# Optimization experiments

Measured on AMD Instinct MI355X. Metric: run time of the kernel, lower is better.

The kernel has to match this reference:

```python
import jax, jax.numpy as jnp
import numpy as np
import math

B, S, D, H = 4, 2048, 1024, 16
HD = D // H  # head_dim = 64


def _rope_tables(max_len, half_dim, theta=10000.0):
    inv_freq = 1.0 / (theta ** (jnp.arange(0, half_dim, dtype=jnp.float32) / half_dim))
    ang = jnp.arange(max_len, dtype=jnp.float32)[:, None] * inv_freq[None, :]  # [max_len, half_dim]
    return jnp.cos(ang), jnp.sin(ang)


def _apply_rope(x, cos, sin):
    # x: [B, H, S, HD]; cos/sin: [S, HD/2]
    x1, x2 = x[..., ::2], x[..., 1::2]
    # matches torch.cat([x1*cos - x2*sin, x1*sin + x2*cos], dim=-1)
    return jnp.concatenate([x1 * cos - x2 * sin, x1 * sin + x2 * cos], axis=-1)


def setup_inputs() -> dict:
    key = jax.random.key(0)
    kx, kq, ko = jax.random.split(key, 3)
    x = jax.random.normal(kx, (B, S, D), dtype=jnp.float32)
    Wqkv = jax.random.normal(kq, (D, 3 * D), dtype=jnp.float32) / math.sqrt(D)
    Wout = jax.random.normal(ko, (D, D), dtype=jnp.float32) / math.sqrt(D)
    cos, sin = _rope_tables(S, HD // 2)
    # causal additive mask, per-batch as in module signature [B, S, S]
    causal = jnp.where(jnp.tril(jnp.ones((S, S), dtype=bool)), 0.0, -1e9).astype(jnp.float32)
    mask = jnp.broadcast_to(causal, (B, S, S))
    return {"x": x, "cos": cos, "sin": sin, "mask": mask, "Wqkv": Wqkv, "Wout": Wout}


def reference(x, cos, sin, mask, Wqkv, Wout):
    b, s, d = x.shape
    qkv = x @ Wqkv  # [B, S, 3D]
    q, k, v = jnp.split(qkv, 3, axis=-1)
    def to_heads(t):
        return t.reshape(b, s, H, HD).transpose(0, 2, 1, 3)  # [B, H, S, HD]
    q, k, v = to_heads(q), to_heads(k), to_heads(v)
    q = _apply_rope(q, cos[:s], sin[:s])
    k = _apply_rope(k, cos[:s], sin[:s])
    scores = jnp.einsum("bhqd,bhkd->bhqk", q, k) / math.sqrt(HD)
    attn = jax.nn.softmax(scores + mask[:, None, :, :], axis=-1)
    out = jnp.einsum("bhqk,bhkd->bhqd", attn, v)  # [B, H, S, HD]
    out = out.transpose(0, 2, 1, 3).reshape(b, s, d)
    return out @ Wout
```

## Files before the change

### kernel.cpp

```cpp
#include <hip/hip_runtime.h>
#include <hip/hip_bf16.h>
#include <stdint.h>

#define B_   4
#define S_   2048
#define D_   1024
#define H_   16
#define HD_  64
#define BH_  (B_*H_)
#define MROWS (B_*S_)

typedef short  short8  __attribute__((ext_vector_type(8)));
typedef float  floatx4 __attribute__((ext_vector_type(4)));

__device__ __forceinline__ ushort f2bf(float f) {
    union { float f; uint32_t u; } v; v.f = f;
    uint32_t u = v.u;
    return (ushort)((u + 0x7FFFu + ((u >> 16) & 1u)) >> 16);
}
__device__ __forceinline__ float u2f(uint32_t u) {
    union { uint32_t u; float f; } v; v.u = u; return v.f;
}
__device__ __forceinline__ uint32_t f2u(float f) {
    union { float f; uint32_t u; } v; v.f = f; return v.u;
}

__device__ __forceinline__ void gl_lds16(const ushort* g, ushort* l) {
    __builtin_amdgcn_global_load_lds(
        (const __attribute__((address_space(1))) unsigned int*)g,
        (__attribute__((address_space(3))) unsigned int*)l,
        16, 0, 0);
}

__global__ __launch_bounds__(256)
void k_prep(const float* __restrict__ x, const float* __restrict__ Wqkv,
            const float* __restrict__ Wout,
            ushort* __restrict__ Xbf, ushort* __restrict__ WqkvT, ushort* __restrict__ WoutT) {
    __shared__ float tile[32][33];
    int blk = blockIdx.x;
    int tid = threadIdx.x;
    if (blk >= 4096) {
        int i = (blk - 4096) * 1024 + tid * 4;
        float4 f = *(const float4*)(x + i);
        ushort4 o; o.x = f2bf(f.x); o.y = f2bf(f.y); o.z = f2bf(f.z); o.w = f2bf(f.w);
        *(ushort4*)(Xbf + i) = o;
        return;
    }
    const float* in; ushort* out; int R, C, bx, by;
    if (blk < 3072) { in = Wqkv; out = WqkvT; R = D_; C = 3 * D_; bx = (blk % 96) * 32; by = (blk / 96) * 32; }
    else            { int b2 = blk - 3072; in = Wout; out = WoutT; R = D_; C = D_; bx = (b2 % 32) * 32; by = (b2 / 32) * 32; }
    int tx = tid & 31, ty = tid >> 5;
    #pragma unroll
    for (int j = 0; j < 32; j += 8)
        tile[ty + j][tx] = in[(size_t)(by + ty + j) * C + bx + tx];
    __syncthreads();
    #pragma unroll
    for (int j = 0; j < 32; j += 8)
        out[(size_t)(bx + ty + j) * R + by + tx] = f2bf(tile[tx][ty + j]);
}

#define BM 128
#define BN 128
#define BK 64

template<int EPI>
__global__ __launch_bounds__(256)
void k_gemm(const ushort* __restrict__ A, const ushort* __restrict__ Bt,
            float* __restrict__ outF,
            ushort* __restrict__ q_out, ushort* __restrict__ k_out, ushort* __restrict__ v_out,
            int M, int N, int K) {
    __shared__ __align__(16) ushort As[BM * 64];
    __shared__ __align__(16) ushort Bs[BN * 64];
    int tid  = threadIdx.x;
    int lane = tid & 63;
    int wave = tid >> 6;
    int quad = lane >> 4;
    int l16  = lane & 15;
    int bm = blockIdx.y * BM;
    int bn = blockIdx.x * BN;
    int wm = (wave >> 1) * 64;
    int wn = (wave & 1) * 64;

    floatx4 acc[4][4] = {};

    for (int k0 = 0; k0 < K; k0 += BK) {
        __syncthreads();
        #pragma unroll
        for (int i = 0; i < 4; i++) {
            int c   = i * 256 + tid;
            int row = c >> 3;
            int gc  = (c & 7) ^ (row & 7);
            gl_lds16(&A[(size_t)(bm + row) * K + k0 + gc * 8],  &As[c * 8]);
            gl_lds16(&Bt[(size_t)(bn + row) * K + k0 + gc * 8], &Bs[c * 8]);
        }
        __syncthreads();
        #pragma unroll
        for (int kk = 0; kk < 2; kk++) {
            short8 af[4], bf[4];
            #pragma unroll
            for (int mt = 0; mt < 4; mt++)
                af[mt] = *(const short8*)&As[(wm + mt * 16 + l16) * 64 +
                                             (((kk * 4 + quad) ^ (l16 & 7)) << 3)];
            #pragma unroll
            for (int nt = 0; nt < 4; nt++)
                bf[nt] = *(const short8*)&Bs[(wn + nt * 16 + l16) * 64 +
                                             (((kk * 4 + quad) ^ (l16 & 7)) << 3)];
            #pragma unroll
            for (int mt = 0; mt < 4; mt++)
                #pragma unroll
                for (int nt = 0; nt < 4; nt++)
                    acc[mt][nt] = __builtin_amdgcn_mfma_f32_16x16x32_bf16(af[mt], bf[nt], acc[mt][nt], 0, 0, 0);
        }
    }

    #pragma unroll
    for (int mt = 0; mt < 4; mt++)
        #pragma unroll
        for (int nt = 0; nt < 4; nt++)
            #pragma unroll
            for (int r = 0; r < 4; r++) {
                int row = bm + wm + mt * 16 + quad * 4 + r;
                int col = bn + wn + nt * 16 + l16;
                float v = acc[mt][nt][r];
                if (EPI == 0) {
                    int which = col >> 10;
                    int rem   = col & 1023;
                    int h  = rem >> 6, hd = rem & 63;
                    int b  = row >> 11, s  = row & 2047;
                    size_t idx = ((size_t)(b * H_ + h) * S_ + s) * HD_ + hd;
                    ushort bv = f2bf(v);
                    ushort* dst = (which == 0) ? q_out : (which == 1) ? k_out : v_out;
                    dst[idx] = bv;
                } else {
                    outF[(size_t)row * N + col] = v;
                }
            }
}

__global__ __launch_bounds__(256)
void k_ropevt(ushort* __restrict__ Q, ushort* __restrict__ Kv,
              const ushort* __restrict__ Vb, ushort* __restrict__ VbT,
              const float* __restrict__ cosT, const float* __restrict__ sinT) {
    __shared__ __align__(16) ushort t[64 * 72];
    int blk = blockIdx.x;
    int tid = threadIdx.x;
    if (blk < 32768) {
        int wid  = (blk * 256 + tid) >> 6;
        int lane = tid & 63;
        int s  = wid & (S_ - 1);
        int bh = wid >> 11;
        int i  = lane & 31;
        float c  = cosT[s * 32 + i];
        float sn = sinT[s * 32 + i];
        size_t base = ((size_t)bh * S_ + s) * HD_;

        uint32_t uq = *(const uint32_t*)&Q[base + 2 * i];
        float x1 = u2f(uq << 16), x2 = u2f(uq & 0xFFFF0000u);
        float o  = (lane < 32) ? (x1 * c - x2 * sn) : (x1 * sn + x2 * c);
        Q[base + lane] = f2bf(o * 0.1803368801f);

        uint32_t uk = *(const uint32_t*)&Kv[base + 2 * i];
        x1 = u2f(uk << 16); x2 = u2f(uk & 0xFFFF0000u);
        o  = (lane < 32) ? (x1 * c - x2 * sn) : (x1 * sn + x2 * c);
        Kv[base + lane] = f2bf(o);
        return;
    }
    int b2 = blk - 32768;
    int bh = b2 >> 5;
    int s0 = (b2 & 31) * 64;
    int ss = tid >> 2, c0 = (tid & 3) * 16;
    size_t base = (size_t)bh * S_ * HD_;
    *(uint4*)&t[ss * 72 + c0]     = *(const uint4*)&Vb[base + (size_t)(s0 + ss) * HD_ + c0];
    *(uint4*)&t[ss * 72 + c0 + 8] = *(const uint4*)&Vb[base + (size_t)(s0 + ss) * HD_ + c0 + 8];
    __syncthreads();
    int hd = tid >> 2, q0 = (tid & 3) * 16;
    ushort tmp[16];
    #pragma unroll
    for (int e = 0; e < 16; e++) tmp[e] = t[(q0 + e) * 72 + hd];
    size_t obase = (size_t)bh * HD_ * S_ + (size_t)hd * S_ + s0 + q0;
    *(uint4*)&VbT[obase]     = *(const uint4*)&tmp[0];
    *(uint4*)&VbT[obase + 8] = *(const uint4*)&tmp[8];
}

__global__ __launch_bounds__(256, 4)
void k_attn(const ushort* __restrict__ Q, const ushort* __restrict__ K,
            const ushort* __restrict__ VT, ushort* __restrict__ O) {
    __shared__ __align__(16) ushort Ks[64 * 64];
    __shared__ __align__(16) ushort Vt[64 * 64];
    __shared__ __align__(16) ushort Pst[4][32 * 64];

    int tid  = threadIdx.x;
    int lane = tid & 63;
    int wave = tid >> 6;
    int quad = lane >> 4;
    int l16  = lane & 15;

    int bh   = blockIdx.x & 63;
    int p    = blockIdx.x >> 6;
    int sA   = p;
    int sB   = 31 - p;
    size_t hbase = (size_t)bh * S_ * HD_;
    size_t vbase = (size_t)bh * HD_ * S_;

    int mrow[2] = { sA * 64 + wave * 16, sB * 64 + wave * 16 };

    short8 qf[2][2];
    #pragma unroll
    for (int m = 0; m < 2; m++)
        #pragma unroll
        for (int h = 0; h < 2; h++)
            qf[m][h] = *(const short8*)&Q[hbase + (size_t)(mrow[m] + l16) * HD_ + quad * 8 + h * 32];

    short8 ones;
    #pragma unroll
    for (int e = 0; e < 8; e++) ones[e] = (short)0x3F80;

    floatx4 acc[2][4] = {};
    floatx4 accl[2] = {};
    const floatx4 z4 = {0.f, 0.f, 0.f, 0.f};

    int c0r = tid >> 3;
    int c1r = (256 + tid) >> 3;
    const ushort* kp0 = &K[hbase + (size_t)c0r * HD_ + (((tid & 7) ^ (c0r & 7)) << 3)];
    const ushort* kp1 = &K[hbase + (size_t)c1r * HD_ + (((tid & 7) ^ (c1r & 7)) << 3)];
    const ushort* vp0 = &VT[vbase + (size_t)c0r * S_ + (((tid & 7) ^ (c0r & 7)) << 3)];
    const ushort* vp1 = &VT[vbase + (size_t)c1r * S_ + (((tid & 7) ^ (c1r & 7)) << 3)];

    int nk = sB + 1;

    uint4 rk0 = *(const uint4*)kp0;
    uint4 rk1 = *(const uint4*)kp1;
    uint4 rv0 = *(const uint4*)vp0;
    uint4 rv1 = *(const uint4*)vp1;
    kp0 += 64 * HD_; kp1 += 64 * HD_; vp0 += 64; vp1 += 64;

    for (int kb = 0; kb < nk; kb++) {
        int k0 = kb * 64;
        __syncthreads();
        *(uint4*)&Ks[tid * 8]         = rk0;
        *(uint4*)&Ks[(256 + tid) * 8] = rk1;
        *(uint4*)&Vt[tid * 8]         = rv0;
        *(uint4*)&Vt[(256 + tid) * 8] = rv1;
        if (kb + 1 < nk) {
            rk0 = *(const uint4*)kp0;
            rk1 = *(const uint4*)kp1;
            rv0 = *(const uint4*)vp0;
            rv1 = *(const uint4*)vp1;
            kp0 += 64 * HD_; kp1 += 64 * HD_; vp0 += 64; vp1 += 64;
        }
        __syncthreads();

        bool act0 = (k0 <= mrow[0] + 15);

        #pragma unroll
        for (int kt = 0; kt < 4; kt++) {
            short8 kf0 = *(const short8*)&Ks[(kt * 16 + l16) * 64 + ((quad ^ (l16 & 7)) << 3)];
            short8 kf1 = *(const short8*)&Ks[(kt * 16 + l16) * 64 + (((4 + quad) ^ (l16 & 7)) << 3)];

            __builtin_amdgcn_s_setprio(1);
            floatx4 s1 = __builtin_amdgcn_mfma_f32_16x16x32_bf16(kf0, qf[1][0], z4, 0, 0, 0);
            s1         = __builtin_amdgcn_mfma_f32_16x16x32_bf16(kf1, qf[1][1], s1, 0, 0, 0);
            floatx4 s0 = z4;
            if (act0) {
                s0 = __builtin_amdgcn_mfma_f32_16x16x32_bf16(kf0, qf[0][0], z4, 0, 0, 0);
                s0 = __builtin_amdgcn_mfma_f32_16x16x32_bf16(kf1, qf[0][1], s0, 0, 0, 0);
            }
            __builtin_amdgcn_s_setprio(0);

            int pc = (kt * 4 + quad) ^ (l16 & 14);
            #pragma unroll
            for (int m = 0; m < 2; m++) {
                if (m == 0 && !act0) continue;
                floatx4 sm = (m == 0) ? s0 : s1;
                bool needMask = (k0 + 63 > mrow[m]);
                int qr = mrow[m] + l16;
                float pp[4];
                #pragma unroll
                for (int r = 0; r < 4; r++) {
                    float v = __builtin_amdgcn_exp2f(sm[r]);
                    if (needMask) {
                        int kc = k0 + kt * 16 + quad * 4 + r;
                        if (kc > qr) v = 0.0f;
                    }
                    pp[r] = v;
                }
                uint2 pk;
                asm("v_cvt_pk_bf16_f32 %0, %1, %2" : "=v"(pk.x) : "v"(pp[0]), "v"(pp[1]));
                asm("v_cvt_pk_bf16_f32 %0, %1, %2" : "=v"(pk.y) : "v"(pp[2]), "v"(pp[3]));
                *(uint2*)&Pst[wave][(m * 16 + l16) * 64 + pc * 4] = pk;
            }
        }

        bool act[2] = { act0, true };
        #pragma unroll
        for (int k2 = 0; k2 < 2; k2++) {
            short8 vb[4];
            #pragma unroll
            for (int nt = 0; nt < 4; nt++)
                vb[nt] = *(const short8*)&Vt[(nt * 16 + l16) * 64 +
                                             (((k2 * 4 + quad) ^ (l16 & 7)) << 3)];
            int pe = (k2 * 8 + quad * 2) ^ (l16 & 14);
            __builtin_amdgcn_s_setprio(1);
            #pragma unroll
            for (int m = 0; m < 2; m++) {
                if (!act[m]) continue;
                short8 pa = *(const short8*)&Pst[wave][(m * 16 + l16) * 64 + pe * 4];
                #pragma unroll
                for (int nt = 0; nt < 4; nt++)
                    acc[m][nt] = __builtin_amdgcn_mfma_f32_16x16x32_bf16(pa, vb[nt], acc[m][nt], 0, 0, 0);
                accl[m] = __builtin_amdgcn_mfma_f32_16x16x32_bf16(pa, ones, accl[m], 0, 0, 0);
            }
            __builtin_amdgcn_s_setprio(0);
        }
    }

    int b = bh >> 4, h = bh & 15;
    #pragma unroll
    for (int m = 0; m < 2; m++)
        #pragma unroll
        for (int r = 0; r < 4; r++) {
            float inv = __builtin_amdgcn_rcpf(accl[m][r]);
            int qr = mrow[m] + quad * 4 + r;
            #pragma unroll
            for (int nt = 0; nt < 4; nt++)
                O[((size_t)(b * S_ + qr)) * D_ + h * HD_ + nt * 16 + l16] = f2bf(acc[m][nt][r] * inv);
        }
}

extern "C" void kernel_launch(void* const* d_in, const int* in_sizes, int n_in,
                              void* d_out, int out_size, void* d_ws, size_t ws_size,
                              hipStream_t stream) {
    const float* x    = (const float*)d_in[0];
    const float* cosT = (const float*)d_in[1];
    const float* sinT = (const float*)d_in[2];
    const float* Wqkv = (const float*)d_in[4];
    const float* Wout = (const float*)d_in[5];
    float* out = (float*)d_out;

    ushort* ws = (ushort*)d_ws;
    ushort* Xbf    = ws;
    ushort* WqkvT  = Xbf    + (size_t)MROWS * D_;
    ushort* WoutT  = WqkvT  + (size_t)3 * D_ * D_;
    ushort* Qb     = WoutT  + (size_t)D_ * D_;
    ushort* Kb     = Qb     + (size_t)BH_ * S_ * HD_;
    ushort* Vb     = Kb     + (size_t)BH_ * S_ * HD_;
    ushort* VbT    = Vb     + (size_t)BH_ * S_ * HD_;
    ushort* AO     = Xbf;

    k_prep<<<12288, 256, 0, stream>>>(x, Wqkv, Wout, Xbf, WqkvT, WoutT);
    k_gemm<0><<<dim3(3 * D_ / BN, MROWS / BM), 256, 0, stream>>>(Xbf, WqkvT, nullptr, Qb, Kb, Vb,
                                                                 MROWS, 3 * D_, D_);
    k_ropevt<<<34816, 256, 0, stream>>>(Qb, Kb, Vb, VbT, cosT, sinT);
    k_attn<<<1024, 256, 0, stream>>>(Qb, Kb, VbT, AO);
    k_gemm<1><<<dim3(D_ / BN, MROWS / BM), 256, 0, stream>>>(AO, WoutT, out, nullptr, nullptr, nullptr,
                                                             MROWS, D_, D_);
}
```

Measured before the change: 294.4 us.

## Fuse RoPE and Q scaling into QKV GEMM epilogue via LDS-staged vector stores

```diff
diff --git a/kernel.cpp b/kernel.cpp
--- a/kernel.cpp
+++ b/kernel.cpp
@@ -68,9 +68,11 @@
 void k_gemm(const ushort* __restrict__ A, const ushort* __restrict__ Bt,
             float* __restrict__ outF,
             ushort* __restrict__ q_out, ushort* __restrict__ k_out, ushort* __restrict__ v_out,
-            int M, int N, int K) {
-    __shared__ __align__(16) ushort As[BM * 64];
-    __shared__ __align__(16) ushort Bs[BN * 64];
+            int M, int N, int K,
+            const float* __restrict__ cosT, const float* __restrict__ sinT) {
+    __shared__ __align__(16) ushort smem[128 * 132];
+    ushort* As = smem;
+    ushort* Bs = smem + BM * 64;
     int tid  = threadIdx.x;
     int lane = tid & 63;
     int wave = tid >> 6;
@@ -113,61 +115,89 @@
         }
     }
 
+    if (EPI == 1) {
+        #pragma unroll
+        for (int mt = 0; mt < 4; mt++)
+            #pragma unroll
+            for (int nt = 0; nt < 4; nt++)
+                #pragma unroll
+                for (int r = 0; r < 4; r++) {
+                    int row = bm + wm + mt * 16 + quad * 4 + r;
+                    int col = bn + wn + nt * 16 + l16;
+                    outF[(size_t)row * N + col] = acc[mt][nt][r];
+                }
+        return;
+    }
+
+    __syncthreads();
     #pragma unroll
     for (int mt = 0; mt < 4; mt++)
         #pragma unroll
         for (int nt = 0; nt < 4; nt++)
             #pragma unroll
             for (int r = 0; r < 4; r++) {
-                int row = bm + wm + mt * 16 + quad * 4 + r;
-                int col = bn + wn + nt * 16 + l16;
-                float v = acc[mt][nt][r];
-                if (EPI == 0) {
-                    int which = col >> 10;
-                    int rem   = col & 1023;
-                    int h  = rem >> 6, hd = rem & 63;
-                    int b  = row >> 11, s  = row & 2047;
-                    size_t idx = ((size_t)(b * H_ + h) * S_ + s) * HD_ + hd;
-                    ushort bv = f2bf(v);
-                    ushort* dst = (which == 0) ? q_out : (which == 1) ? k_out : v_out;
-                    dst[idx] = bv;
-                } else {
-                    outF[(size_t)row * N + col] = v;
-                }
-            }
+                int srow = wm + mt * 16 + quad * 4 + r;
+                int scol = wn + nt * 16 + l16;
+                smem[srow * 132 + scol] = f2bf(acc[mt][nt][r]);
+            }
+    __syncthreads();
+
+    int which = bn >> 10;
+    ushort* dst = (which == 0) ? q_out : (which == 1) ? k_out : v_out;
+    int hbase2 = (bn & 1023) >> 6;
+
+    #pragma unroll
+    for (int i = 0; i < 8; i++) {
+        int g    = i * 256 + tid;
+        int srow = g >> 4;
+        int cc   = (g & 15) * 8;
+        int s    = bm + srow;
+        int b    = s >> 11, sloc = s & 2047;
+        int h    = hbase2 + (cc >> 6);
+        int hd0  = cc & 63;
+        size_t didx = ((size_t)((b * H_ + h) * S_ + sloc)) * HD_ + hd0;
+
+        if (which == 2) {
+            uint2 a0 = *(const uint2*)&smem[srow * 132 + cc];
+            uint2 a1 = *(const uint2*)&smem[srow * 132 + cc + 4];
+            uint4 o4 = make_uint4(a0.x, a0.y, a1.x, a1.y);
+            *(uint4*)&dst[didx] = o4;
+        } else {
+            int  i0 = cc & 31;
+            bool up = (cc & 32) != 0;
+            int  cb = cc & ~63;
+            const ushort* in = &smem[srow * 132 + cb + 2 * i0];
+            uint2 wA = *(const uint2*)&in[0];
+            uint2 wB = *(const uint2*)&in[4];
+            uint2 wC = *(const uint2*)&in[8];
+            uint2 wD = *(const uint2*)&in[12];
+            uint32_t w[8] = { wA.x, wA.y, wB.x, wB.y, wC.x, wC.y, wD.x, wD.y };
+            float cs[8], sn[8];
+            *(float4*)&cs[0] = *(const float4*)&cosT[sloc * 32 + i0];
+            *(float4*)&cs[4] = *(const float4*)&cosT[sloc * 32 + i0 + 4];
+            *(float4*)&sn[0] = *(const float4*)&sinT[sloc * 32 + i0];
+            *(float4*)&sn[4] = *(const float4*)&sinT[sloc * 32 + i0 + 4];
+            ushort o[8];
+            #pragma unroll
+            for (int e = 0; e < 8; e++) {
+                float x1 = u2f(w[e] << 16);
+                float x2 = u2f(w[e] & 0xFFFF0000u);
+                float ov = up ? (x1 * sn[e] + x2 * cs[e]) : (x1 * cs[e] - x2 * sn[e]);
+                if (which == 0) ov *= 0.1803368801f;
+                o[e] = f2bf(ov);
+            }
+            *(uint4*)&dst[didx] = *(uint4*)o;
+        }
+    }
 }
 
 __global__ __launch_bounds__(256)
-void k_ropevt(ushort* __restrict__ Q, ushort* __restrict__ Kv,
-              const ushort* __restrict__ Vb, ushort* __restrict__ VbT,
-              const float* __restrict__ cosT, const float* __restrict__ sinT) {
+void k_vt(const ushort* __restrict__ Vb, ushort* __restrict__ VbT) {
     __shared__ __align__(16) ushort t[64 * 72];
     int blk = blockIdx.x;
     int tid = threadIdx.x;
-    if (blk < 32768) {
-        int wid  = (blk * 256 + tid) >> 6;
-        int lane = tid & 63;
-        int s  = wid & (S_ - 1);
-        int bh = wid >> 11;
-        int i  = lane & 31;
-        float c  = cosT[s * 32 + i];
-        float sn = sinT[s * 32 + i];
-        size_t base = ((size_t)bh * S_ + s) * HD_;
-
-        uint32_t uq = *(const uint32_t*)&Q[base + 2 * i];
-        float x1 = u2f(uq << 16), x2 = u2f(uq & 0xFFFF0000u);
-        float o  = (lane < 32) ? (x1 * c - x2 * sn) : (x1 * sn + x2 * c);
-        Q[base + lane] = f2bf(o * 0.1803368801f);
-
-        uint32_t uk = *(const uint32_t*)&Kv[base + 2 * i];
-        x1 = u2f(uk << 16); x2 = u2f(uk & 0xFFFF0000u);
-        o  = (lane < 32) ? (x1 * c - x2 * sn) : (x1 * sn + x2 * c);
-        Kv[base + lane] = f2bf(o);
-        return;
-    }
-    int b2 = blk - 32768;
-    int bh = b2 >> 5;
-    int s0 = (b2 & 31) * 64;
+    int bh = blk >> 5;
+    int s0 = (blk & 31) * 64;
     int ss = tid >> 2, c0 = (tid & 3) * 16;
     size_t base = (size_t)bh * S_ * HD_;
     *(uint4*)&t[ss * 72 + c0]     = *(const uint4*)&Vb[base + (size_t)(s0 + ss) * HD_ + c0];
@@ -349,9 +379,9 @@
 
     k_prep<<<12288, 256, 0, stream>>>(x, Wqkv, Wout, Xbf, WqkvT, WoutT);
     k_gemm<0><<<dim3(3 * D_ / BN, MROWS / BM), 256, 0, stream>>>(Xbf, WqkvT, nullptr, Qb, Kb, Vb,
-                                                                 MROWS, 3 * D_, D_);
-    k_ropevt<<<34816, 256, 0, stream>>>(Qb, Kb, Vb, VbT, cosT, sinT);
+                                                                 MROWS, 3 * D_, D_, cosT, sinT);
+    k_vt<<<2048, 256, 0, stream>>>(Vb, VbT);
     k_attn<<<1024, 256, 0, stream>>>(Qb, Kb, VbT, AO);
     k_gemm<1><<<dim3(D_ / BN, MROWS / BM), 256, 0, stream>>>(AO, WoutT, out, nullptr, nullptr, nullptr,
-                                                             MROWS, D_, D_);
-}
+                                                             MROWS, D_, D_, nullptr, nullptr);
+}
```

Measured after the change: 290.7 us. About the same (-1.2%).
